# Kernel tuning notes

Measured on AMD Instinct MI355X. Metric: run time of the kernel, lower is better.

Reference implementation:

```python
import jax, jax.numpy as jnp
import numpy as np

# Model hyperparameters (match init_kwargs)
B, REF_P, IN_P, OUT_P = 32, 256, 256, 256
K, KS = 4, 3
RATIO = 0.25
HIDDEN = int(REF_P * RATIO) + 1  # 65, per canonical attention1d
TEMP = 34.0
STRIDE, PAD, DIL, GROUPS = 1, 1, 1, 1
L, L_REF = 4096, 64


def setup_inputs() -> dict:
    key = jax.random.key(0)
    k0, k1, k2, k3, k4 = jax.random.split(key, 5)
    ref = jax.random.normal(k0, (B, REF_P, L_REF), dtype=jnp.float32)
    x = jax.random.normal(k1, (B, IN_P, L), dtype=jnp.float32)
    # attention1d params: fc1 (1x1 conv, no bias), fc2 (1x1 conv, with bias)
    att_w1 = jax.random.normal(k2, (HIDDEN, REF_P), dtype=jnp.float32) * (1.0 / np.sqrt(REF_P))
    att_w2 = jax.random.normal(k3, (K, HIDDEN), dtype=jnp.float32) * (1.0 / np.sqrt(HIDDEN))
    att_b2 = jnp.zeros((K,), dtype=jnp.float32)
    # kaiming-uniform-ish K-bank of conv kernels: [K, out, in/groups, ks]
    fan_in = (IN_P // GROUPS) * KS
    bound = np.sqrt(6.0 / fan_in)
    weight = jax.random.uniform(k4, (K, OUT_P, IN_P // GROUPS, KS), dtype=jnp.float32,
                                minval=-bound, maxval=bound)
    bias = jnp.zeros((K, OUT_P), dtype=jnp.float32)
    return {"ref": ref, "x": x, "att_w1": att_w1, "att_w2": att_w2,
            "att_b2": att_b2, "weight": weight, "bias": bias}


def reference(ref, x, att_w1, att_w2, att_b2, weight, bias):
    b = x.shape[0]
    # attention1d: global avg pool over length, two 1x1 convs, softmax w/ temperature
    pooled = jnp.mean(ref, axis=-1)                       # [B, REF_P]
    h = jax.nn.relu(pooled @ att_w1.T)                    # [B, HIDDEN]
    logits = h @ att_w2.T + att_b2                        # [B, K]
    attn = jax.nn.softmax(logits / TEMP, axis=1)          # [B, K]
    # aggregate per-sample kernel bank
    agg_w = jnp.einsum('bk,koic->boic', attn, weight)     # [B, OUT, IN/g, KS]
    agg_b = attn @ bias                                   # [B, OUT]
    # batched grouped conv1d, exactly as F.conv1d with groups=B*GROUPS
    xr = x.reshape(1, b * IN_P, -1)                       # [1, B*IN, L]
    wr = agg_w.reshape(b * OUT_P, IN_P // GROUPS, KS)     # [B*OUT, IN/g, KS]
    out = jax.lax.conv_general_dilated(
        xr, wr, window_strides=(STRIDE,), padding=[(PAD, PAD)],
        rhs_dilation=(DIL,), dimension_numbers=('NCH', 'OIH', 'NCH'),
        feature_group_count=b * GROUPS)                   # [1, B*OUT, L_out]
    out = out.reshape(b, OUT_P, -1) + agg_b[:, :, None]
    return out
```

## Files before the change

kernel.cpp:

```cpp
#include <hip/hip_runtime.h>
#include <cstdint>
#include <cstddef>

typedef __bf16 bf16;
typedef bf16 bf16x8 __attribute__((ext_vector_type(8)));
typedef float f32x4 __attribute__((ext_vector_type(4)));

typedef __attribute__((address_space(1))) void as1_void;
typedef __attribute__((address_space(3))) void as3_void;

__device__ __forceinline__ void gload16(const void* g, void* l) {
  __builtin_amdgcn_global_load_lds((const as1_void*)g, (as3_void*)l, 16, 0, 0);
}

__global__ __launch_bounds__(256) void attn_kernel(
    const float* __restrict__ ref, const float* __restrict__ w1,
    const float* __restrict__ w2, const float* __restrict__ b2,
    const float* __restrict__ bias, float* __restrict__ attn,
    float* __restrict__ aggb) {
  const int b = blockIdx.x, t = threadIdx.x;
  __shared__ float pooled[256];
  __shared__ float hsh[65];
  __shared__ float ash[4];
  {
    const float* r = ref + ((size_t)b * 256 + t) * 64;
    float s = 0.f;
    #pragma unroll
    for (int l = 0; l < 64; l += 4) {
      float4 v = *(const float4*)(r + l);
      s += v.x + v.y + v.z + v.w;
    }
    pooled[t] = s * (1.0f / 64.0f);
  }
  __syncthreads();
  if (t < 65) {
    const float* w = w1 + t * 256;
    float s = 0.f;
    for (int p = 0; p < 256; ++p) s += pooled[p] * w[p];
    hsh[t] = fmaxf(s, 0.f);
  }
  __syncthreads();
  if (t == 0) {
    float lg[4];
    for (int k = 0; k < 4; ++k) {
      float s = b2[k];
      for (int j = 0; j < 65; ++j) s += hsh[j] * w2[k * 65 + j];
      lg[k] = s * (1.0f / 34.0f);
    }
    float m = fmaxf(fmaxf(lg[0], lg[1]), fmaxf(lg[2], lg[3]));
    float e[4], se = 0.f;
    for (int k = 0; k < 4; ++k) { e[k] = expf(lg[k] - m); se += e[k]; }
    float inv = 1.0f / se;
    for (int k = 0; k < 4; ++k) { float a = e[k] * inv; ash[k] = a; attn[b * 4 + k] = a; }
  }
  __syncthreads();
  {
    float s = 0.f;
    for (int k = 0; k < 4; ++k) s += ash[k] * bias[k * 256 + t];
    aggb[b * 256 + t] = s;
  }
}

__global__ __launch_bounds__(256) void aggw_kernel(
    const float* __restrict__ weight, const float* __restrict__ attn,
    bf16* __restrict__ Wagg) {
  const int o = blockIdx.x, b = blockIdx.y, i = threadIdx.x;
  const float a0 = attn[b * 4 + 0], a1 = attn[b * 4 + 1];
  const float a2 = attn[b * 4 + 2], a3 = attn[b * 4 + 3];
  const size_t ks = (size_t)256 * 256 * 3;
  const float* w = weight + ((size_t)o * 256 + i) * 3;
  bf16* dst = Wagg + ((size_t)(b * 256 + o)) * 768 + i;
  #pragma unroll
  for (int s = 0; s < 3; ++s) {
    float v = a0 * w[s] + a1 * w[ks + s] + a2 * w[2 * ks + s] + a3 * w[3 * ks + s];
    dst[s * 256] = (bf16)v;
  }
}

__global__ __launch_bounds__(256) void conv_kernel(
    const float* __restrict__ x, const bf16* __restrict__ Wagg,
    const float* __restrict__ aggb, float* __restrict__ out) {
  __shared__ bf16 Wl[2][128 * 64];
  __shared__ bf16 Xl[130 * 64];
  const int tid = threadIdx.x;
  const int lane = tid & 63, wid = tid >> 6;
  const int bid = blockIdx.x;
  const int swz = (bid & 7) * 256 + (bid >> 3);
  const int b  = swz >> 6;
  const int ot = (swz >> 5) & 1;
  const int lt = swz & 31;
  const int l0 = lt * 128, o0 = ot * 128;
  const int wm = wid >> 1, wn = wid & 1;
  const float* xb = x + (size_t)b * 256 * 4096;
  const bf16* Wb = Wagg + ((size_t)(b * 256 + o0)) * 768;
  f32x4 acc[4][4] = {};

  auto stage_w = [&](int step, int buf) {
    const int s = step % 3, ib = step / 3;
    const int koff = s * 256 + ib * 64;
    #pragma unroll
    for (int r = 0; r < 4; ++r) {
      int c = r * 256 + tid;
      int row = c >> 3, subg = (c & 7) ^ (row & 7);
      gload16(Wb + (size_t)row * 768 + koff + subg * 8,
              (char*)&Wl[buf][0] + (r * 256 + wid * 64) * 16);
    }
  };

  const int sg = tid >> 5, lc = tid & 31;
  const float* xmain = xb + ((size_t)sg * 8) * 4096 + l0 + lc * 4;
  const int eg = (tid >> 1) & 7;
  const int erow = (tid & 1) ? 129 : 0;
  const int el = (tid & 1) ? (l0 + 128) : (l0 - 1);
  const bool edge_ok = (el >= 0) && (el < 4096);

  float4 xv[8];
  float ev[8];

  auto load_x = [&](int ib) {
    const float* p = xmain + (size_t)ib * 64 * 4096;
    #pragma unroll
    for (int r = 0; r < 8; ++r)
      xv[r] = *(const float4*)(p + (size_t)r * 4096);
    if (tid < 16) {
      #pragma unroll
      for (int r = 0; r < 8; ++r)
        ev[r] = edge_ok ? xb[(size_t)(ib * 64 + eg * 8 + r) * 4096 + el] : 0.f;
    }
  };
  auto write_x = [&]() {
    char* base = (char*)&Xl[0];
    #pragma unroll
    for (int q = 0; q < 4; ++q) {
      const int row = lc * 4 + 1 + q;
      bf16x8 pk;
      #pragma unroll
      for (int r = 0; r < 8; ++r) pk[r] = (bf16)(((const float*)&xv[r])[q]);
      *(bf16x8*)(base + row * 128 + ((sg ^ (row & 7)) << 4)) = pk;
    }
    if (tid < 16) {
      bf16x8 pe;
      #pragma unroll
      for (int r = 0; r < 8; ++r) pe[r] = (bf16)ev[r];
      *(bf16x8*)(base + erow * 128 + ((eg ^ (erow & 7)) << 4)) = pe;
    }
  };

  load_x(0);
  stage_w(0, 0);
  write_x();
  __syncthreads();

  for (int ib = 0; ib < 4; ++ib) {
    if (ib < 3) load_x(ib + 1);
    const char* xbuf = (const char*)&Xl[0];
    #pragma unroll
    for (int s = 0; s < 3; ++s) {
      const int step = ib * 3 + s;
      if (step < 11) stage_w(step + 1, (step + 1) & 1);
      const char* wbuf = (const char*)&Wl[step & 1][0];
      #pragma unroll
      for (int kk = 0; kk < 2; ++kk) {
        const int sub = (lane >> 4) + kk * 4;
        bf16x8 af[4], bfr[4];
        #pragma unroll
        for (int m = 0; m < 4; ++m) {
          int row = wm * 64 + m * 16 + (lane & 15);
          af[m] = *(const bf16x8*)(wbuf + row * 128 + ((sub ^ (row & 7)) << 4));
        }
        #pragma unroll
        for (int n = 0; n < 4; ++n) {
          int row = wn * 64 + n * 16 + (lane & 15) + s;
          bfr[n] = *(const bf16x8*)(xbuf + row * 128 + ((sub ^ (row & 7)) << 4));
        }
        #pragma unroll
        for (int m = 0; m < 4; ++m)
          #pragma unroll
          for (int n = 0; n < 4; ++n)
            acc[m][n] = __builtin_amdgcn_mfma_f32_16x16x32_bf16(af[m], bfr[n], acc[m][n], 0, 0, 0);
      }
      if (step < 11) __syncthreads();
    }
    if (ib < 3) {
      write_x();
      __syncthreads();
    }
  }

  const int b256 = b * 256;
  #pragma unroll
  for (int m = 0; m < 4; ++m) {
    const int ob = o0 + wm * 64 + m * 16 + ((lane >> 4) << 2);
    float bb[4];
    #pragma unroll
    for (int r = 0; r < 4; ++r) bb[r] = aggb[b256 + ob + r];
    #pragma unroll
    for (int n = 0; n < 4; ++n) {
      const int l = l0 + wn * 64 + n * 16 + (lane & 15);
      f32x4 v = acc[m][n];
      #pragma unroll
      for (int r = 0; r < 4; ++r)
        out[((size_t)(b256 + ob + r)) * 4096 + l] = v[r] + bb[r];
    }
  }
}

extern "C" void kernel_launch(void* const* d_in, const int* in_sizes, int n_in,
                              void* d_out, int out_size, void* d_ws, size_t ws_size,
                              hipStream_t stream) {
  const float* ref    = (const float*)d_in[0];
  const float* x      = (const float*)d_in[1];
  const float* w1     = (const float*)d_in[2];
  const float* w2     = (const float*)d_in[3];
  const float* b2     = (const float*)d_in[4];
  const float* weight = (const float*)d_in[5];
  const float* bias   = (const float*)d_in[6];
  float* out = (float*)d_out;
  char* ws = (char*)d_ws;

  const size_t WAGG_BYTES = (size_t)32 * 256 * 768 * 2;
  bf16* Wagg  = (bf16*)ws;
  float* attn = (float*)(ws + WAGG_BYTES);
  float* aggb = (float*)(ws + WAGG_BYTES + 512);

  attn_kernel<<<32, 256, 0, stream>>>(ref, w1, w2, b2, bias, attn, aggb);
  aggw_kernel<<<dim3(256, 32), 256, 0, stream>>>(weight, attn, Wagg);
  conv_kernel<<<2048, 256, 0, stream>>>(x, Wagg, aggb, out);
}
```

Baseline: 105.3 us.

## Triple-buffer weight tiles in conv kernel with explicit vmcnt waits and barriers

The conv kernel's weight LDS staging grows from two buffers to three, so each of the three kernel-tap slices has a fixed slot. The main loop is restructured into explicit per-tap blocks that issue weight loads two steps ahead. The old full __syncthreads per step is replaced by s_waitcnt vmcnt plus a raw s_barrier, aiming to hide global-to-LDS latency and cut sync stalls. The extra buffer raises LDS use per block, which may lower occupancy. Correctness now depends on the manual waitcnt accounting for the async LDS loads.

```diff
diff --git a/kernel.cpp b/kernel.cpp
--- a/kernel.cpp
+++ b/kernel.cpp
@@ -12,6 +12,10 @@
 __device__ __forceinline__ void gload16(const void* g, void* l) {
   __builtin_amdgcn_global_load_lds((const as1_void*)g, (as3_void*)l, 16, 0, 0);
 }
+#define SBAR()   do { __builtin_amdgcn_s_barrier(); \
+                      __builtin_amdgcn_sched_barrier(0); } while (0)
+#define VMCNT(n) do { asm volatile("s_waitcnt vmcnt(" #n ")" ::: "memory"); \
+                      __builtin_amdgcn_sched_barrier(0); } while (0)
 
 __global__ __launch_bounds__(256) void attn_kernel(
     const float* __restrict__ ref, const float* __restrict__ w1,
@@ -80,7 +84,7 @@
 __global__ __launch_bounds__(256) void conv_kernel(
     const float* __restrict__ x, const bf16* __restrict__ Wagg,
     const float* __restrict__ aggb, float* __restrict__ out) {
-  __shared__ bf16 Wl[2][128 * 64];
+  __shared__ bf16 Wl[3][128 * 64];
   __shared__ bf16 Xl[130 * 64];
   const int tid = threadIdx.x;
   const int lane = tid & 63, wid = tid >> 6;
@@ -95,15 +99,15 @@
   const bf16* Wb = Wagg + ((size_t)(b * 256 + o0)) * 768;
   f32x4 acc[4][4] = {};
 
-  auto stage_w = [&](int step, int buf) {
-    const int s = step % 3, ib = step / 3;
-    const int koff = s * 256 + ib * 64;
+  auto stage_w = [&](int t, int slot) {
+    const int ss = t % 3, ibb = t / 3;
+    const int koff = ss * 256 + ibb * 64;
     #pragma unroll
     for (int r = 0; r < 4; ++r) {
       int c = r * 256 + tid;
       int row = c >> 3, subg = (c & 7) ^ (row & 7);
       gload16(Wb + (size_t)row * 768 + koff + subg * 8,
-              (char*)&Wl[buf][0] + (r * 256 + wid * 64) * 16);
+              (char*)&Wl[slot][0] + (r * 256 + wid * 64) * 16);
     }
   };
 
@@ -146,46 +150,60 @@
     }
   };
 
+  auto kkblock = [&](int s, int slot) {
+    const char* wbuf = (const char*)&Wl[slot][0];
+    const char* xbuf = (const char*)&Xl[0];
+    #pragma unroll
+    for (int kk = 0; kk < 2; ++kk) {
+      const int sub = (lane >> 4) + kk * 4;
+      bf16x8 af[4], bfr[4];
+      #pragma unroll
+      for (int m = 0; m < 4; ++m) {
+        int row = wm * 64 + m * 16 + (lane & 15);
+        af[m] = *(const bf16x8*)(wbuf + row * 128 + ((sub ^ (row & 7)) << 4));
+      }
+      #pragma unroll
+      for (int n = 0; n < 4; ++n) {
+        int row = wn * 64 + n * 16 + (lane & 15) + s;
+        bfr[n] = *(const bf16x8*)(xbuf + row * 128 + ((sub ^ (row & 7)) << 4));
+      }
+      #pragma unroll
+      for (int m = 0; m < 4; ++m)
+        #pragma unroll
+        for (int n = 0; n < 4; ++n)
+          acc[m][n] = __builtin_amdgcn_mfma_f32_16x16x32_bf16(af[m], bfr[n], acc[m][n], 0, 0, 0);
+    }
+  };
+
   load_x(0);
   stage_w(0, 0);
+  stage_w(1, 1);
   write_x();
   __syncthreads();
 
-  for (int ib = 0; ib < 4; ++ib) {
-    if (ib < 3) load_x(ib + 1);
-    const char* xbuf = (const char*)&Xl[0];
-    #pragma unroll
-    for (int s = 0; s < 3; ++s) {
-      const int step = ib * 3 + s;
-      if (step < 11) stage_w(step + 1, (step + 1) & 1);
-      const char* wbuf = (const char*)&Wl[step & 1][0];
-      #pragma unroll
-      for (int kk = 0; kk < 2; ++kk) {
-        const int sub = (lane >> 4) + kk * 4;
-        bf16x8 af[4], bfr[4];
-        #pragma unroll
-        for (int m = 0; m < 4; ++m) {
-          int row = wm * 64 + m * 16 + (lane & 15);
-          af[m] = *(const bf16x8*)(wbuf + row * 128 + ((sub ^ (row & 7)) << 4));
-        }
-        #pragma unroll
-        for (int n = 0; n < 4; ++n) {
-          int row = wn * 64 + n * 16 + (lane & 15) + s;
-          bfr[n] = *(const bf16x8*)(xbuf + row * 128 + ((sub ^ (row & 7)) << 4));
-        }
-        #pragma unroll
-        for (int m = 0; m < 4; ++m)
-          #pragma unroll
-          for (int n = 0; n < 4; ++n)
-            acc[m][n] = __builtin_amdgcn_mfma_f32_16x16x32_bf16(af[m], bfr[n], acc[m][n], 0, 0, 0);
-      }
-      if (step < 11) __syncthreads();
-    }
-    if (ib < 3) {
-      write_x();
-      __syncthreads();
-    }
-  }
+  for (int J = 0; J < 3; ++J) {
+    stage_w(J * 3 + 2, 2);
+    kkblock(0, 0);
+    VMCNT(4);
+    SBAR();
+    stage_w(J * 3 + 3, 0);
+    kkblock(1, 1);
+    VMCNT(4);
+    SBAR();
+    load_x(J + 1);
+    stage_w(J * 3 + 4, 1);
+    kkblock(2, 2);
+    __syncthreads();
+    write_x();
+    __syncthreads();
+  }
+
+  stage_w(11, 2);
+  kkblock(0, 0);
+  kkblock(1, 1);
+  VMCNT(0);
+  SBAR();
+  kkblock(2, 2);
 
   const int b256 = b * 256;
   #pragma unroll
```

After: 114.0 us. 8.3% more time.
